# Performance work log

Hardware: AMD Instinct MI355X
Metric: run time of the kernel (lower is better)

Reference implementation:

```python
import jax, jax.numpy as jnp
import numpy as np

B, C, D, H, W = 2, 64, 12, 256, 64


def _conv1x1_relu(x, w, b):
    # x: (B, C, D, H, W); w: (C_out, C_in); b: (C_out,)
    y = jnp.einsum('oc,bcdhw->bodhw', w, x) + b[None, :, None, None, None]
    return jax.nn.relu(y)


def setup_inputs() -> dict:
    key = jax.random.key(0)
    ks = jax.random.split(key, 9)
    s = 1.0 / np.sqrt(C)
    inp = {
        'rep': jax.random.normal(ks[0], (B, C, D, H, W), dtype=jnp.float32),
        'Wq_w': jax.random.normal(ks[1], (C, C), dtype=jnp.float32) * s,
        'Wq_b': jnp.zeros((C,), dtype=jnp.float32),
        'Wk_w': jax.random.normal(ks[2], (C, C), dtype=jnp.float32) * s,
        'Wk_b': jnp.zeros((C,), dtype=jnp.float32),
        'Wv_w': jax.random.normal(ks[3], (C, C), dtype=jnp.float32) * s,
        'Wv_b': jnp.zeros((C,), dtype=jnp.float32),
        'FC_w': jax.random.normal(ks[4], (C, C), dtype=jnp.float32) * s,
        'FC_b': jnp.zeros((C,), dtype=jnp.float32),
    }
    return inp


def reference(rep, Wq_w, Wq_b, Wk_w, Wk_b, Wv_w, Wv_b, FC_w, FC_b):
    # 1x1x1 conv projections + ReLU, then permute to (B, D, W, H, C)
    q = _conv1x1_relu(rep, Wq_w, Wq_b).transpose(0, 2, 4, 3, 1)
    k = _conv1x1_relu(rep, Wk_w, Wk_b).transpose(0, 2, 4, 3, 1)
    v = _conv1x1_relu(rep, Wv_w, Wv_b).transpose(0, 2, 4, 3, 1)
    # attention over H axis: scores (B, D, W, H, H)
    scores = jnp.einsum('bdwhc,bdwgc->bdwhg', q, k) / jnp.sqrt(jnp.asarray(C, rep.dtype))
    attn = jax.nn.softmax(scores, axis=-1)
    out = jnp.einsum('bdwhg,bdwgc->bdwhc', attn, v)
    # permute(0,4,1,3,2): (B, D, W, H, C) -> (B, C, D, H, W)
    out = out.transpose(0, 4, 1, 3, 2)
    return _conv1x1_relu(out, FC_w, FC_b)
```

## Files before the change

kernel.cpp:

```cpp
#include <hip/hip_runtime.h>

typedef float f32x4 __attribute__((ext_vector_type(4)));
typedef short bf16x8 __attribute__((ext_vector_type(8)));
typedef unsigned short ushort_t;

#define NB 2
#define NC 64
#define ND 12
#define NH 256
#define NW 64
#define CSTRIDE (ND*NH*NW)
#define QSZ_ELEMS (24*64*256*64)
#define WS_NEED   ((size_t)3*QSZ_ELEMS*2)

__device__ __forceinline__ ushort_t bf_round(float f){
    unsigned int u = __float_as_uint(f);
    return (ushort_t)((u + 0x7fffu + ((u >> 16) & 1u)) >> 16);
}
__device__ __forceinline__ float bf_to_f(ushort_t s){ return __uint_as_float(((unsigned int)s) << 16); }

union U4S8 { uint4 u; bf16x8 s; };

__device__ __forceinline__ int row64_off(int r, int o){
    return r*128 + ((((o>>3) ^ (r&7)))<<4) + (o&7)*2;
}
__device__ __forceinline__ int row64_chunk(int r, int kchunk){
    return r*128 + (((kchunk ^ (r&7)))<<4);
}
__device__ __forceinline__ int vt_off(int c, int g){
    return c*512 + ((((g>>3) ^ (c&7)))<<4) + (g&7)*2;
}
__device__ __forceinline__ int vt_chunk(int c, int gchunk){
    return c*512 + (((gchunk ^ (c&7)))<<4);
}

__device__ __forceinline__ U4S8 wfrag_f(const float* W, int hl, int G, int ot, int m){
    const float* p2 = W + (hl + 16*ot)*NC + 32*m + 8*G;
    float4 f0 = *(const float4*)p2;
    float4 f1 = *(const float4*)(p2 + 4);
    U4S8 u; ushort_t* s = (ushort_t*)&u;
    s[0]=bf_round(f0.x); s[1]=bf_round(f0.y); s[2]=bf_round(f0.z); s[3]=bf_round(f0.w);
    s[4]=bf_round(f1.x); s[5]=bf_round(f1.y); s[6]=bf_round(f1.z); s[7]=bf_round(f1.w);
    return u;
}

__global__ __launch_bounds__(256, 2) void k1_proj(
    const float* __restrict__ rep,
    const float* __restrict__ Wq, const float* __restrict__ bq,
    const float* __restrict__ Wk, const float* __restrict__ bk,
    const float* __restrict__ Wv, const float* __restrict__ bv,
    ushort_t* __restrict__ qws, ushort_t* __restrict__ kws, ushort_t* __restrict__ vws)
{
    __shared__ __align__(16) unsigned char XL[32768];

    const int t = threadIdx.x, lane = t & 63, wid = t >> 6;
    const int G = lane >> 4, hl = lane & 15;
    const int blk = blockIdx.x;
    const int bd = blk >> 6;
    const int h0 = (blk & 63) * 4;
    const int d = bd % ND, b = bd / ND;
    const long dbase2 = (long)b*NC*CSTRIDE + (long)d*(NH*NW) + (long)h0*NW;

#pragma unroll
    for (int oct = 0; oct < 8; ++oct){
        float f[8];
#pragma unroll
        for (int j = 0; j < 8; ++j)
            f[j] = rep[dbase2 + (long)(8*oct + j)*CSTRIDE + t];
        U4S8 u; ushort_t* s = (ushort_t*)&u;
#pragma unroll
        for (int j = 0; j < 8; ++j) s[j] = bf_round(f[j]);
        *(uint4*)(XL + row64_chunk(t, oct)) = u.u;
    }
    __syncthreads();

    U4S8 xa[4][2];
#pragma unroll
    for (int nt = 0; nt < 4; ++nt)
#pragma unroll
        for (int m = 0; m < 2; ++m)
            xa[nt][m].u = *(const uint4*)(XL + row64_chunk(64*wid + 16*nt + hl, 4*m + G));
    __syncthreads();

    auto pass = [&](const float* W, const float* bias, float scale, ushort_t* dst){
        U4S8 bw[4][2];
        float bb[4];
#pragma unroll
        for (int ot = 0; ot < 4; ++ot){
            bw[ot][0] = wfrag_f(W, hl, G, ot, 0);
            bw[ot][1] = wfrag_f(W, hl, G, ot, 1);
            bb[ot] = bias[hl + 16*ot];
        }
        f32x4 acc[4][4];
#pragma unroll
        for (int nt = 0; nt < 4; ++nt)
#pragma unroll
            for (int ot = 0; ot < 4; ++ot){
                f32x4 a = {0.f,0.f,0.f,0.f};
                a = __builtin_amdgcn_mfma_f32_16x16x32_bf16(xa[nt][0].s, bw[ot][0].s, a, 0,0,0);
                a = __builtin_amdgcn_mfma_f32_16x16x32_bf16(xa[nt][1].s, bw[ot][1].s, a, 0,0,0);
#pragma unroll
                for (int r = 0; r < 4; ++r) a[r] = fmaxf(a[r] + bb[ot], 0.f) * scale;
                acc[nt][ot] = a;
            }
#pragma unroll
        for (int nt = 0; nt < 4; ++nt)
#pragma unroll
            for (int ot = 0; ot < 4; ++ot)
#pragma unroll
                for (int r = 0; r < 4; ++r){
                    int n = 64*wid + 16*nt + 4*G + r;
                    int o = hl + 16*ot;
                    *(ushort_t*)(XL + row64_off(n, o)) = bf_round(acc[nt][ot][r]);
                }
        __syncthreads();
#pragma unroll
        for (int i = 0; i < 8; ++i){
            int g2 = i*256 + t; int n = g2 >> 3; int c8 = g2 & 7;
            uint4 u = *(const uint4*)(XL + row64_chunk(n, c8));
            long row_g = ((long)bd*64 + (n & 63))*256 + h0 + (n >> 6);
            *(uint4*)((unsigned char*)dst + row_g*128 + c8*16) = u;
        }
        __syncthreads();
    };
    pass(Wq, bq, 0.125f, qws);
    pass(Wk, bk, 1.0f,   kws);
    pass(Wv, bv, 1.0f,   vws);
}

__global__ __launch_bounds__(256, 2) void k2_attn(
    ushort_t* __restrict__ qws, const ushort_t* __restrict__ kws, const ushort_t* __restrict__ vws)
{
    __shared__ __align__(16) unsigned char smem[65536];
    unsigned char* KL = smem;
    unsigned char* VT = smem + 32768;

    const int t = threadIdx.x, lane = t & 63, wid = t >> 6;
    const int G = lane >> 4, hl = lane & 15;
    const int bdw = blockIdx.x;
    ushort_t* qslice = qws + (size_t)bdw*16384;
    const unsigned char* kslice = (const unsigned char*)(kws + (size_t)bdw*16384);
    const unsigned char* vslice = (const unsigned char*)(vws + (size_t)bdw*16384);

#pragma unroll
    for (int i = 0; i < 8; ++i){
        int g2 = i*256 + t; int g = g2 >> 3; int c8 = g2 & 7;
        uint4 ku = *(const uint4*)(kslice + g2*16);
        *(uint4*)(KL + row64_chunk(g, c8)) = ku;
        U4S8 vu; vu.u = *(const uint4*)(vslice + g2*16);
#pragma unroll
        for (int j = 0; j < 8; ++j)
            *(ushort_t*)(VT + vt_off(8*c8 + j, g)) = (ushort_t)vu.s[j];
    }
    __syncthreads();

    U4S8 qfr[4][2];
#pragma unroll
    for (int ht = 0; ht < 4; ++ht)
#pragma unroll
        for (int m = 0; m < 2; ++m)
            qfr[ht][m].u = *(const uint4*)((const unsigned char*)qslice
                              + (64*wid + 16*ht + hl)*128 + (4*m + G)*16);

    f32x4 oacc[4][4];
#pragma unroll
    for (int ct = 0; ct < 4; ++ct)
#pragma unroll
        for (int ht = 0; ht < 4; ++ht) oacc[ct][ht] = (f32x4){0.f,0.f,0.f,0.f};
    float m_run[4], l_run[4];
#pragma unroll
    for (int ht = 0; ht < 4; ++ht){ m_run[ht] = -1e30f; l_run[ht] = 0.f; }

    const int srcq0 = (16*((2*G    ) & 3) + hl)*4;
    const int srcq1 = (16*((2*G + 1) & 3) + hl)*4;

    for (int gb = 0; gb < NH; gb += 64){
        U4S8 kfr[4][2];
#pragma unroll
        for (int gt = 0; gt < 4; ++gt)
#pragma unroll
            for (int m = 0; m < 2; ++m)
                kfr[gt][m].u = *(const uint4*)(KL + row64_chunk(gb + 16*gt + hl, 4*m + G));

        f32x4 sacc[4][4];
#pragma unroll
        for (int gt = 0; gt < 4; ++gt)
#pragma unroll
            for (int ht = 0; ht < 4; ++ht){
                f32x4 a = {0.f,0.f,0.f,0.f};
                a = __builtin_amdgcn_mfma_f32_16x16x32_bf16(kfr[gt][0].s, qfr[ht][0].s, a, 0,0,0);
                a = __builtin_amdgcn_mfma_f32_16x16x32_bf16(kfr[gt][1].s, qfr[ht][1].s, a, 0,0,0);
                sacc[gt][ht] = a;
            }

        unsigned int pk[4][4][2];
#pragma unroll
        for (int ht = 0; ht < 4; ++ht){
            float cm = -1e30f;
#pragma unroll
            for (int gt = 0; gt < 4; ++gt)
#pragma unroll
                for (int r = 0; r < 4; ++r) cm = fmaxf(cm, sacc[gt][ht][r]);
            cm = fmaxf(cm, __shfl_xor(cm, 16));
            cm = fmaxf(cm, __shfl_xor(cm, 32));
            const float mn  = fmaxf(m_run[ht], cm);
            const float corr = __expf(m_run[ht] - mn);
            m_run[ht] = mn;
            float ls = 0.f;
#pragma unroll
            for (int gt = 0; gt < 4; ++gt){
                f32x4 s = sacc[gt][ht];
                float e0 = __expf(s[0]-mn), e1 = __expf(s[1]-mn);
                float e2 = __expf(s[2]-mn), e3 = __expf(s[3]-mn);
                ls += (e0+e1)+(e2+e3);
                pk[ht][gt][0] = (unsigned int)bf_round(e0) | ((unsigned int)bf_round(e1) << 16);
                pk[ht][gt][1] = (unsigned int)bf_round(e2) | ((unsigned int)bf_round(e3) << 16);
            }
            ls += __shfl_xor(ls, 16);
            ls += __shfl_xor(ls, 32);
            l_run[ht] = l_run[ht]*corr + ls;
#pragma unroll
            for (int ct = 0; ct < 4; ++ct)
#pragma unroll
                for (int r = 0; r < 4; ++r) oacc[ct][ht][r] *= corr;
        }

        U4S8 vfr[4][2];
#pragma unroll
        for (int ct = 0; ct < 4; ++ct)
#pragma unroll
            for (int m = 0; m < 2; ++m)
                vfr[ct][m].u = *(const uint4*)(VT + vt_chunk(16*ct + hl, (gb>>3) + 4*m + G));

#pragma unroll
        for (int m = 0; m < 2; ++m){
            U4S8 bfr[4];
#pragma unroll
            for (int ht = 0; ht < 4; ++ht){
                unsigned int wv[4];
#pragma unroll
                for (int jj = 0; jj < 4; ++jj){
                    const int src = (jj >> 1) ? srcq1 : srcq0;
                    const int p2  = jj & 1;
                    int rA = __builtin_amdgcn_ds_bpermute(src, (int)pk[ht][2*m  ][p2]);
                    int rB = __builtin_amdgcn_ds_bpermute(src, (int)pk[ht][2*m+1][p2]);
                    wv[jj] = (lane < 32) ? (unsigned int)rA : (unsigned int)rB;
                }
                bfr[ht].u = make_uint4(wv[0], wv[1], wv[2], wv[3]);
            }
#pragma unroll
            for (int ct = 0; ct < 4; ++ct)
#pragma unroll
                for (int ht = 0; ht < 4; ++ht)
                    oacc[ct][ht] = __builtin_amdgcn_mfma_f32_16x16x32_bf16(vfr[ct][m].s, bfr[ht].s, oacc[ct][ht], 0,0,0);
        }
    }

    float invl[4];
#pragma unroll
    for (int ht = 0; ht < 4; ++ht) invl[ht] = 1.f / l_run[ht];

    __syncthreads();
#pragma unroll
    for (int ct = 0; ct < 4; ++ct)
#pragma unroll
        for (int ht = 0; ht < 4; ++ht)
#pragma unroll
            for (int r = 0; r < 4; ++r){
                int h = 64*wid + 16*ht + hl;
                int c = 16*ct + 4*G + r;
                *(ushort_t*)(KL + row64_off(h, c)) = bf_round(oacc[ct][ht][r] * invl[ht]);
            }
    __syncthreads();
#pragma unroll
    for (int i = 0; i < 8; ++i){
        int g2 = i*256 + t;
        uint4 u = *(const uint4*)(KL + row64_chunk(g2 >> 3, g2 & 7));
        *(uint4*)((unsigned char*)qslice + g2*16) = u;
    }
}

__global__ __launch_bounds__(256, 2) void k3_fc(
    const ushort_t* __restrict__ ows, const float* __restrict__ Wf, const float* __restrict__ bfc,
    float* __restrict__ out)
{
    __shared__ __align__(16) float YL[16384];

    const int t = threadIdx.x, lane = t & 63, wid = t >> 6;
    const int G = lane >> 4, hl = lane & 15;
    const int blk = blockIdx.x;
    const int bd = blk >> 6;
    const int h0 = (blk & 63) * 4;
    const int d = bd % ND, b = bd / ND;

    U4S8 xa[4][2];
#pragma unroll
    for (int nt = 0; nt < 4; ++nt)
#pragma unroll
        for (int m = 0; m < 2; ++m){
            long row_g = ((long)bd*64 + (16*nt + hl))*256 + h0 + wid;
            xa[nt][m].u = *(const uint4*)((const unsigned char*)ows + row_g*128 + (4*m + G)*16);
        }

    U4S8 bw[4][2];
    float bb[4];
#pragma unroll
    for (int ot = 0; ot < 4; ++ot){
        bw[ot][0] = wfrag_f(Wf, hl, G, ot, 0);
        bw[ot][1] = wfrag_f(Wf, hl, G, ot, 1);
        bb[ot] = bfc[hl + 16*ot];
    }

    f32x4 acc[4][4];
#pragma unroll
    for (int nt = 0; nt < 4; ++nt)
#pragma unroll
        for (int ot = 0; ot < 4; ++ot){
            f32x4 a = {0.f,0.f,0.f,0.f};
            a = __builtin_amdgcn_mfma_f32_16x16x32_bf16(xa[nt][0].s, bw[ot][0].s, a, 0,0,0);
            a = __builtin_amdgcn_mfma_f32_16x16x32_bf16(xa[nt][1].s, bw[ot][1].s, a, 0,0,0);
#pragma unroll
            for (int r = 0; r < 4; ++r) a[r] = fmaxf(a[r] + bb[ot], 0.f);
            acc[nt][ot] = a;
        }

#pragma unroll
    for (int nt = 0; nt < 4; ++nt)
#pragma unroll
        for (int ot = 0; ot < 4; ++ot)
#pragma unroll
            for (int r = 0; r < 4; ++r){
                int n = 64*wid + 16*nt + 4*G + r;
                int o = hl + 16*ot;
                YL[(n<<6) + (o ^ ((n>>2)&31))] = acc[nt][ot][r];
            }
    __syncthreads();

    const long base3 = (long)b*NC*CSTRIDE + (long)d*(NH*NW) + (long)h0*NW;
#pragma unroll
    for (int i = 0; i < 16; ++i){
        int idx = i*1024 + t*4;
        int o = idx >> 8;
        int n0 = idx & 255;
        int osw = o ^ (t & 31);
        float4 v;
        v.x = YL[((n0+0)<<6) + osw];
        v.y = YL[((n0+1)<<6) + osw];
        v.z = YL[((n0+2)<<6) + osw];
        v.w = YL[((n0+3)<<6) + osw];
        *(float4*)(&out[base3 + (long)o*CSTRIDE + n0]) = v;
    }
}

__global__ __launch_bounds__(256, 2) void sa_mfma(
    const float* __restrict__ rep,
    const float* __restrict__ Wq, const float* __restrict__ bq,
    const float* __restrict__ Wk, const float* __restrict__ bk,
    const float* __restrict__ Wv, const float* __restrict__ bv,
    const float* __restrict__ Wf, const float* __restrict__ bfc,
    float* __restrict__ out)
{
    __shared__ __align__(16) unsigned char smem[65536];
    unsigned char* BUFA = smem;
    unsigned char* BUFB = smem + 32768;

    const int t = threadIdx.x, lane = t & 63, wid = t >> 6;
    const int G = lane >> 4, hl = lane & 15;
    const int j = blockIdx.x;
    const int x = j & 7;
    const int p = j >> 3;
    const int group = ((p >> 6) << 3) + x;
    const int w = p & 63;
    const int d = group % ND;
    const int b = group / ND;
    const long base_bd = (long)b*(NC*CSTRIDE) + (long)d*(NH*NW) + w;

    {
        const int h = t;
        const long rbase = base_bd + (long)h*NW;
#pragma unroll
        for (int c8 = 0; c8 < 8; ++c8){
            U4S8 u;
            ushort_t* s = (ushort_t*)&u;
#pragma unroll
            for (int jj = 0; jj < 8; ++jj)
                s[jj] = bf_round(rep[rbase + (long)(c8*8 + jj)*CSTRIDE]);
            *(uint4*)(BUFB + row64_chunk(h, c8)) = u.u;
        }
    }
    U4S8 xafr[4][2];
#pragma unroll
    for (int ht = 0; ht < 4; ++ht)
#pragma unroll
        for (int m = 0; m < 2; ++m)
            xafr[ht][m].u = *(const uint4*)(BUFB + row64_chunk(64*wid + 16*ht + hl, 4*m + G));

    auto do_proj = [&](const float* W, const float* bias, float scale, f32x4 (&acc)[4][4]){
        U4S8 bw[4][2];
#pragma unroll
        for (int ot = 0; ot < 4; ++ot){ bw[ot][0] = wfrag_f(W, hl, G, ot, 0); bw[ot][1] = wfrag_f(W, hl, G, ot, 1); }
        float bb[4];
#pragma unroll
        for (int ot = 0; ot < 4; ++ot) bb[ot] = bias[hl + 16*ot];
#pragma unroll
        for (int ht = 0; ht < 4; ++ht)
#pragma unroll
            for (int ot = 0; ot < 4; ++ot){
                f32x4 a = {0.f, 0.f, 0.f, 0.f};
                a = __builtin_amdgcn_mfma_f32_16x16x32_bf16(xafr[ht][0].s, bw[ot][0].s, a, 0, 0, 0);
                a = __builtin_amdgcn_mfma_f32_16x16x32_bf16(xafr[ht][1].s, bw[ot][1].s, a, 0, 0, 0);
#pragma unroll
                for (int r = 0; r < 4; ++r) a[r] = fmaxf(a[r] + bb[ot], 0.f) * scale;
                acc[ht][ot] = a;
            }
    };

    {
        f32x4 qa[4][4];
        do_proj(Wq, bq, 0.125f, qa);
#pragma unroll
        for (int ht = 0; ht < 4; ++ht)
#pragma unroll
            for (int ot = 0; ot < 4; ++ot)
#pragma unroll
                for (int r = 0; r < 4; ++r){
                    int h = 64*wid + 16*ht + 4*G + r;
                    int o = hl + 16*ot;
                    *(ushort_t*)(BUFA + row64_off(h, o)) = bf_round(qa[ht][ot][r]);
                }
    }
    U4S8 qfr[4][2];
#pragma unroll
    for (int ht = 0; ht < 4; ++ht)
#pragma unroll
        for (int m = 0; m < 2; ++m)
            qfr[ht][m].u = *(const uint4*)(BUFA + row64_chunk(64*wid + 16*ht + hl, 4*m + G));

    {
        f32x4 ka[4][4];
        do_proj(Wk, bk, 1.0f, ka);
#pragma unroll
        for (int gt = 0; gt < 4; ++gt)
#pragma unroll
            for (int ot = 0; ot < 4; ++ot)
#pragma unroll
                for (int r = 0; r < 4; ++r){
                    int g = 64*wid + 16*gt + 4*G + r;
                    int o = hl + 16*ot;
                    *(ushort_t*)(BUFA + row64_off(g, o)) = bf_round(ka[gt][ot][r]);
                }
    }
    f32x4 va[4][4];
    do_proj(Wv, bv, 1.0f, va);
    __syncthreads();
#pragma unroll
    for (int gt = 0; gt < 4; ++gt)
#pragma unroll
        for (int ot = 0; ot < 4; ++ot)
#pragma unroll
            for (int r = 0; r < 4; ++r){
                int g = 64*wid + 16*gt + 4*G + r;
                int c = hl + 16*ot;
                *(ushort_t*)(BUFB + vt_off(c, g)) = bf_round(va[gt][ot][r]);
            }
    __syncthreads();

    f32x4 oacc[4][4];
#pragma unroll
    for (int ct = 0; ct < 4; ++ct)
#pragma unroll
        for (int ht = 0; ht < 4; ++ht) oacc[ct][ht] = (f32x4){0.f,0.f,0.f,0.f};
    float m_run[4], l_run[4];
#pragma unroll
    for (int ht = 0; ht < 4; ++ht){ m_run[ht] = -1e30f; l_run[ht] = 0.f; }

    const int srcq0 = (16*((2*G    ) & 3) + hl)*4;
    const int srcq1 = (16*((2*G + 1) & 3) + hl)*4;

    for (int gb = 0; gb < NH; gb += 64){
        U4S8 kfr[4][2];
#pragma unroll
        for (int gt = 0; gt < 4; ++gt)
#pragma unroll
            for (int m = 0; m < 2; ++m)
                kfr[gt][m].u = *(const uint4*)(BUFA + row64_chunk(gb + 16*gt + hl, 4*m + G));

        f32x4 sacc[4][4];
#pragma unroll
        for (int gt = 0; gt < 4; ++gt)
#pragma unroll
            for (int ht = 0; ht < 4; ++ht){
                f32x4 a = {0.f,0.f,0.f,0.f};
                a = __builtin_amdgcn_mfma_f32_16x16x32_bf16(kfr[gt][0].s, qfr[ht][0].s, a, 0,0,0);
                a = __builtin_amdgcn_mfma_f32_16x16x32_bf16(kfr[gt][1].s, qfr[ht][1].s, a, 0,0,0);
                sacc[gt][ht] = a;
            }

        unsigned int pk[4][4][2];
#pragma unroll
        for (int ht = 0; ht < 4; ++ht){
            float cm = -1e30f;
#pragma unroll
            for (int gt = 0; gt < 4; ++gt)
#pragma unroll
                for (int r = 0; r < 4; ++r) cm = fmaxf(cm, sacc[gt][ht][r]);
            cm = fmaxf(cm, __shfl_xor(cm, 16));
            cm = fmaxf(cm, __shfl_xor(cm, 32));
            const float mn  = fmaxf(m_run[ht], cm);
            const float corr = __expf(m_run[ht] - mn);
            m_run[ht] = mn;
            float ls = 0.f;
#pragma unroll
            for (int gt = 0; gt < 4; ++gt){
                f32x4 s = sacc[gt][ht];
                float e0 = __expf(s[0]-mn), e1 = __expf(s[1]-mn);
                float e2 = __expf(s[2]-mn), e3 = __expf(s[3]-mn);
                ls += (e0+e1)+(e2+e3);
                pk[ht][gt][0] = (unsigned int)bf_round(e0) | ((unsigned int)bf_round(e1) << 16);
                pk[ht][gt][1] = (unsigned int)bf_round(e2) | ((unsigned int)bf_round(e3) << 16);
            }
            ls += __shfl_xor(ls, 16);
            ls += __shfl_xor(ls, 32);
            l_run[ht] = l_run[ht]*corr + ls;
#pragma unroll
            for (int ct = 0; ct < 4; ++ct)
#pragma unroll
                for (int r = 0; r < 4; ++r) oacc[ct][ht][r] *= corr;
        }

        U4S8 vfr[4][2];
#pragma unroll
        for (int ct = 0; ct < 4; ++ct)
#pragma unroll
            for (int m = 0; m < 2; ++m)
                vfr[ct][m].u = *(const uint4*)(BUFB + vt_chunk(16*ct + hl, (gb>>3) + 4*m + G));

#pragma unroll
        for (int m = 0; m < 2; ++m){
            U4S8 bfr[4];
#pragma unroll
            for (int ht = 0; ht < 4; ++ht){
                unsigned int wv[4];
#pragma unroll
                for (int jj = 0; jj < 4; ++jj){
                    const int src = (jj >> 1) ? srcq1 : srcq0;
                    const int p2  = jj & 1;
                    int rA = __builtin_amdgcn_ds_bpermute(src, (int)pk[ht][2*m  ][p2]);
                    int rB = __builtin_amdgcn_ds_bpermute(src, (int)pk[ht][2*m+1][p2]);
                    wv[jj] = (lane < 32) ? (unsigned int)rA : (unsigned int)rB;
                }
                bfr[ht].u = make_uint4(wv[0], wv[1], wv[2], wv[3]);
            }
#pragma unroll
            for (int ct = 0; ct < 4; ++ct)
#pragma unroll
                for (int ht = 0; ht < 4; ++ht)
                    oacc[ct][ht] = __builtin_amdgcn_mfma_f32_16x16x32_bf16(vfr[ct][m].s, bfr[ht].s, oacc[ct][ht], 0,0,0);
        }
    }

    float invl[4];
#pragma unroll
    for (int ht = 0; ht < 4; ++ht) invl[ht] = 1.f / l_run[ht];
    __syncthreads();
#pragma unroll
    for (int ct = 0; ct < 4; ++ct)
#pragma unroll
        for (int ht = 0; ht < 4; ++ht)
#pragma unroll
            for (int r = 0; r < 4; ++r){
                float v = oacc[ct][ht][r] * invl[ht];
                ushort_t hi = bf_round(v);
                ushort_t lo = bf_round(v - bf_to_f(hi));
                int hrow = 64*wid + 16*ht + hl;
                int c = 16*ct + 4*G + r;
                *(ushort_t*)(BUFA + row64_off(hrow, c)) = hi;
                *(ushort_t*)(BUFB + row64_off(hrow, c)) = lo;
            }
    U4S8 bh[4][2], bl[4][2];
#pragma unroll
    for (int ht = 0; ht < 4; ++ht)
#pragma unroll
        for (int m = 0; m < 2; ++m){
            bh[ht][m].u = *(const uint4*)(BUFA + row64_chunk(64*wid + 16*ht + hl, 4*m + G));
            bl[ht][m].u = *(const uint4*)(BUFB + row64_chunk(64*wid + 16*ht + hl, 4*m + G));
        }

    f32x4 yacc[4][4];
#pragma unroll
    for (int ot = 0; ot < 4; ++ot)
#pragma unroll
        for (int ht = 0; ht < 4; ++ht) yacc[ot][ht] = (f32x4){0.f,0.f,0.f,0.f};
#pragma unroll
    for (int ot = 0; ot < 4; ++ot)
#pragma unroll
        for (int m = 0; m < 2; ++m){
            U4S8 wf = wfrag_f(Wf, hl, G, ot, m);
#pragma unroll
            for (int ht = 0; ht < 4; ++ht){
                yacc[ot][ht] = __builtin_amdgcn_mfma_f32_16x16x32_bf16(wf.s, bh[ht][m].s, yacc[ot][ht], 0,0,0);
                yacc[ot][ht] = __builtin_amdgcn_mfma_f32_16x16x32_bf16(wf.s, bl[ht][m].s, yacc[ot][ht], 0,0,0);
            }
        }
    float bfv[4][4];
#pragma unroll
    for (int ot = 0; ot < 4; ++ot)
#pragma unroll
        for (int r = 0; r < 4; ++r) bfv[ot][r] = bfc[16*ot + 4*G + r];
#pragma unroll
    for (int ot = 0; ot < 4; ++ot)
#pragma unroll
        for (int ht = 0; ht < 4; ++ht)
#pragma unroll
            for (int r = 0; r < 4; ++r){
                int o = 16*ot + 4*G + r;
                int h = 64*wid + 16*ht + hl;
                float y = fmaxf(yacc[ot][ht][r] + bfv[ot][r], 0.f);
                out[base_bd + (long)o*CSTRIDE + (long)h*NW] = y;
            }
}

extern "C" void kernel_launch(void* const* d_in, const int* in_sizes, int n_in,
                              void* d_out, int out_size, void* d_ws, size_t ws_size,
                              hipStream_t stream) {
    (void)in_sizes; (void)n_in; (void)out_size;
    const float* rep = (const float*)d_in[0];
    const float* Wq  = (const float*)d_in[1];
    const float* bq  = (const float*)d_in[2];
    const float* Wk  = (const float*)d_in[3];
    const float* bk  = (const float*)d_in[4];
    const float* Wv  = (const float*)d_in[5];
    const float* bv  = (const float*)d_in[6];
    const float* Wf  = (const float*)d_in[7];
    const float* bfc = (const float*)d_in[8];
    float* out = (float*)d_out;

    if (ws_size >= WS_NEED) {
        ushort_t* qws = (ushort_t*)d_ws;
        ushort_t* kws = qws + QSZ_ELEMS;
        ushort_t* vws = kws + QSZ_ELEMS;
        k1_proj<<<dim3(1536), dim3(256), 0, stream>>>(rep, Wq, bq, Wk, bk, Wv, bv, qws, kws, vws);
        k2_attn<<<dim3(1536), dim3(256), 0, stream>>>(qws, kws, vws);
        k3_fc  <<<dim3(1536), dim3(256), 0, stream>>>(qws, Wf, bfc, out);
    } else {
        sa_mfma<<<dim3(1536), dim3(256), 0, stream>>>(rep, Wq, bq, Wk, bk, Wv, bv, Wf, bfc, out);
    }
}
```

Before: 174.6 us.

## Double-buffer projection output staging and prefetch weights in projection kernel

The projection kernel now uses a second 32KB LDS buffer so each of the Q, K and V passes writes into an alternating bounce buffer. This drops the barrier between a pass's copy-out and the next pass's MFMA writes. Weight fragments for the next projection are loaded ahead of the current pass to hide global-load latency, and the MFMA epilogue writes straight to LDS without a separate accumulator array. In exchange, LDS per block doubles to 64KB and the occupancy hint in launch_bounds is removed, which may lower the number of resident blocks per CU.

After: 191.8 us. 1.1x slower.

```diff
diff --git a/kernel.cpp b/kernel.cpp
--- a/kernel.cpp
+++ b/kernel.cpp
@@ -44,7 +44,7 @@
     return u;
 }
 
-__global__ __launch_bounds__(256, 2) void k1_proj(
+__global__ __launch_bounds__(256) void k1_proj(
     const float* __restrict__ rep,
     const float* __restrict__ Wq, const float* __restrict__ bq,
     const float* __restrict__ Wk, const float* __restrict__ bk,
@@ -52,6 +52,7 @@
     ushort_t* __restrict__ qws, ushort_t* __restrict__ kws, ushort_t* __restrict__ vws)
 {
     __shared__ __align__(16) unsigned char XL[32768];
+    __shared__ __align__(16) unsigned char OB[32768];
 
     const int t = threadIdx.x, lane = t & 63, wid = t >> 6;
     const int G = lane >> 4, hl = lane & 15;
@@ -60,6 +61,15 @@
     const int h0 = (blk & 63) * 4;
     const int d = bd % ND, b = bd / ND;
     const long dbase2 = (long)b*NC*CSTRIDE + (long)d*(NH*NW) + (long)h0*NW;
+    const long wsrow0 = (long)bd*64*256 + h0;
+
+    U4S8 wqf[4][2]; float bbq[4];
+#pragma unroll
+    for (int ot = 0; ot < 4; ++ot){
+        wqf[ot][0] = wfrag_f(Wq, hl, G, ot, 0);
+        wqf[ot][1] = wfrag_f(Wq, hl, G, ot, 1);
+        bbq[ot] = bq[hl + 16*ot];
+    }
 
 #pragma unroll
     for (int oct = 0; oct < 8; ++oct){
@@ -80,18 +90,9 @@
 #pragma unroll
         for (int m = 0; m < 2; ++m)
             xa[nt][m].u = *(const uint4*)(XL + row64_chunk(64*wid + 16*nt + hl, 4*m + G));
-    __syncthreads();
-
-    auto pass = [&](const float* W, const float* bias, float scale, ushort_t* dst){
-        U4S8 bw[4][2];
-        float bb[4];
-#pragma unroll
-        for (int ot = 0; ot < 4; ++ot){
-            bw[ot][0] = wfrag_f(W, hl, G, ot, 0);
-            bw[ot][1] = wfrag_f(W, hl, G, ot, 1);
-            bb[ot] = bias[hl + 16*ot];
-        }
-        f32x4 acc[4][4];
+
+    auto mfma_pass = [&](U4S8 (&bw)[4][2], float (&bb)[4], float scale,
+                         unsigned char* bounce){
 #pragma unroll
         for (int nt = 0; nt < 4; ++nt)
 #pragma unroll
@@ -100,32 +101,50 @@
                 a = __builtin_amdgcn_mfma_f32_16x16x32_bf16(xa[nt][0].s, bw[ot][0].s, a, 0,0,0);
                 a = __builtin_amdgcn_mfma_f32_16x16x32_bf16(xa[nt][1].s, bw[ot][1].s, a, 0,0,0);
 #pragma unroll
-                for (int r = 0; r < 4; ++r) a[r] = fmaxf(a[r] + bb[ot], 0.f) * scale;
-                acc[nt][ot] = a;
-            }
-#pragma unroll
-        for (int nt = 0; nt < 4; ++nt)
-#pragma unroll
-            for (int ot = 0; ot < 4; ++ot)
-#pragma unroll
                 for (int r = 0; r < 4; ++r){
+                    float v = fmaxf(a[r] + bb[ot], 0.f) * scale;
                     int n = 64*wid + 16*nt + 4*G + r;
                     int o = hl + 16*ot;
-                    *(ushort_t*)(XL + row64_off(n, o)) = bf_round(acc[nt][ot][r]);
+                    *(ushort_t*)(bounce + row64_off(n, o)) = bf_round(v);
                 }
-        __syncthreads();
+            }
+    };
+    auto copyout = [&](const unsigned char* bounce, ushort_t* dst){
 #pragma unroll
         for (int i = 0; i < 8; ++i){
             int g2 = i*256 + t; int n = g2 >> 3; int c8 = g2 & 7;
-            uint4 u = *(const uint4*)(XL + row64_chunk(n, c8));
-            long row_g = ((long)bd*64 + (n & 63))*256 + h0 + (n >> 6);
+            uint4 u = *(const uint4*)(bounce + row64_chunk(n, c8));
+            long row_g = wsrow0 + (long)(n & 63)*256 + (n >> 6);
             *(uint4*)((unsigned char*)dst + row_g*128 + c8*16) = u;
         }
-        __syncthreads();
     };
-    pass(Wq, bq, 0.125f, qws);
-    pass(Wk, bk, 1.0f,   kws);
-    pass(Wv, bv, 1.0f,   vws);
+
+    U4S8 wkf[4][2]; float bbk[4];
+#pragma unroll
+    for (int ot = 0; ot < 4; ++ot){
+        wkf[ot][0] = wfrag_f(Wk, hl, G, ot, 0);
+        wkf[ot][1] = wfrag_f(Wk, hl, G, ot, 1);
+        bbk[ot] = bk[hl + 16*ot];
+    }
+    mfma_pass(wqf, bbq, 0.125f, OB);
+    __syncthreads();
+
+    copyout(OB, qws);
+    U4S8 wvf[4][2]; float bbv[4];
+#pragma unroll
+    for (int ot = 0; ot < 4; ++ot){
+        wvf[ot][0] = wfrag_f(Wv, hl, G, ot, 0);
+        wvf[ot][1] = wfrag_f(Wv, hl, G, ot, 1);
+        bbv[ot] = bv[hl + 16*ot];
+    }
+    mfma_pass(wkf, bbk, 1.0f, XL);
+    __syncthreads();
+
+    copyout(XL, kws);
+    mfma_pass(wvf, bbv, 1.0f, OB);
+    __syncthreads();
+
+    copyout(OB, vws);
 }
 
 __global__ __launch_bounds__(256, 2) void k2_attn(
```

## Split projection kernel into one block per Q/K/V pass with XCD-aware tile mapping

Applied to the files above, without the earlier changes.

The projection kernel now launches three times as many blocks, each computing only one of the Q, K or V projections for a tile instead of all three serially. Block indices are remapped so the three passes of the same tile land on the same XCD, which should let the repeated reads of the input tile hit in that XCD's L2. This adds parallelism and removes two rounds of barriers and LDS staging per block, at the cost of reading and converting the fp32 input three times per tile.

After: 174.8 us. Within noise of the previous version (+0.1%).

```diff
diff --git a/kernel.cpp b/kernel.cpp
--- a/kernel.cpp
+++ b/kernel.cpp
@@ -55,21 +55,41 @@
 
     const int t = threadIdx.x, lane = t & 63, wid = t >> 6;
     const int G = lane >> 4, hl = lane & 15;
-    const int blk = blockIdx.x;
-    const int bd = blk >> 6;
-    const int h0 = (blk & 63) * 4;
+
+    const int j = blockIdx.x;
+    const int xcd = j & 7;
+    const int pos = j >> 3;
+    const int tile = (pos / 3) * 8 + xcd;
+    const int pass = pos % 3;
+
+    const int bd = tile >> 6;
+    const int h0 = (tile & 63) * 4;
     const int d = bd % ND, b = bd / ND;
     const long dbase2 = (long)b*NC*CSTRIDE + (long)d*(NH*NW) + (long)h0*NW;
+    const long wsrow0 = (long)bd*64*256 + h0;
+
+    const float* W; const float* bias; ushort_t* dst; float scale;
+    if (pass == 0)      { W = Wq; bias = bq; dst = qws; scale = 0.125f; }
+    else if (pass == 1) { W = Wk; bias = bk; dst = kws; scale = 1.0f; }
+    else                { W = Wv; bias = bv; dst = vws; scale = 1.0f; }
+
+    U4S8 bw[4][2]; float bb[4];
+#pragma unroll
+    for (int ot = 0; ot < 4; ++ot){
+        bw[ot][0] = wfrag_f(W, hl, G, ot, 0);
+        bw[ot][1] = wfrag_f(W, hl, G, ot, 1);
+        bb[ot] = bias[hl + 16*ot];
+    }
 
 #pragma unroll
     for (int oct = 0; oct < 8; ++oct){
         float f[8];
 #pragma unroll
-        for (int j = 0; j < 8; ++j)
-            f[j] = rep[dbase2 + (long)(8*oct + j)*CSTRIDE + t];
+        for (int jj = 0; jj < 8; ++jj)
+            f[jj] = rep[dbase2 + (long)(8*oct + jj)*CSTRIDE + t];
         U4S8 u; ushort_t* s = (ushort_t*)&u;
 #pragma unroll
-        for (int j = 0; j < 8; ++j) s[j] = bf_round(f[j]);
+        for (int jj = 0; jj < 8; ++jj) s[jj] = bf_round(f[jj]);
         *(uint4*)(XL + row64_chunk(t, oct)) = u.u;
     }
     __syncthreads();
@@ -82,50 +102,30 @@
             xa[nt][m].u = *(const uint4*)(XL + row64_chunk(64*wid + 16*nt + hl, 4*m + G));
     __syncthreads();
 
-    auto pass = [&](const float* W, const float* bias, float scale, ushort_t* dst){
-        U4S8 bw[4][2];
-        float bb[4];
+#pragma unroll
+    for (int nt = 0; nt < 4; ++nt)
 #pragma unroll
         for (int ot = 0; ot < 4; ++ot){
-            bw[ot][0] = wfrag_f(W, hl, G, ot, 0);
-            bw[ot][1] = wfrag_f(W, hl, G, ot, 1);
-            bb[ot] = bias[hl + 16*ot];
-        }
-        f32x4 acc[4][4];
-#pragma unroll
-        for (int nt = 0; nt < 4; ++nt)
-#pragma unroll
-            for (int ot = 0; ot < 4; ++ot){
-                f32x4 a = {0.f,0.f,0.f,0.f};
-                a = __builtin_amdgcn_mfma_f32_16x16x32_bf16(xa[nt][0].s, bw[ot][0].s, a, 0,0,0);
-                a = __builtin_amdgcn_mfma_f32_16x16x32_bf16(xa[nt][1].s, bw[ot][1].s, a, 0,0,0);
-#pragma unroll
-                for (int r = 0; r < 4; ++r) a[r] = fmaxf(a[r] + bb[ot], 0.f) * scale;
-                acc[nt][ot] = a;
-            }
-#pragma unroll
-        for (int nt = 0; nt < 4; ++nt)
-#pragma unroll
-            for (int ot = 0; ot < 4; ++ot)
-#pragma unroll
-                for (int r = 0; r < 4; ++r){
-                    int n = 64*wid + 16*nt + 4*G + r;
-                    int o = hl + 16*ot;
-                    *(ushort_t*)(XL + row64_off(n, o)) = bf_round(acc[nt][ot][r]);
-                }
-        __syncthreads();
-#pragma unroll
-        for (int i = 0; i < 8; ++i){
-            int g2 = i*256 + t; int n = g2 >> 3; int c8 = g2 & 7;
-            uint4 u = *(const uint4*)(XL + row64_chunk(n, c8));
-            long row_g = ((long)bd*64 + (n & 63))*256 + h0 + (n >> 6);
-            *(uint4*)((unsigned char*)dst + row_g*128 + c8*16) = u;
-        }
-        __syncthreads();
-    };
-    pass(Wq, bq, 0.125f, qws);
-    pass(Wk, bk, 1.0f,   kws);
-    pass(Wv, bv, 1.0f,   vws);
+            f32x4 a = {0.f,0.f,0.f,0.f};
+            a = __builtin_amdgcn_mfma_f32_16x16x32_bf16(xa[nt][0].s, bw[ot][0].s, a, 0,0,0);
+            a = __builtin_amdgcn_mfma_f32_16x16x32_bf16(xa[nt][1].s, bw[ot][1].s, a, 0,0,0);
+#pragma unroll
+            for (int r = 0; r < 4; ++r){
+                float v = fmaxf(a[r] + bb[ot], 0.f) * scale;
+                int n = 64*wid + 16*nt + 4*G + r;
+                int o = hl + 16*ot;
+                *(ushort_t*)(XL + row64_off(n, o)) = bf_round(v);
+            }
+        }
+    __syncthreads();
+
+#pragma unroll
+    for (int i = 0; i < 8; ++i){
+        int g2 = i*256 + t; int n = g2 >> 3; int c8 = g2 & 7;
+        uint4 u = *(const uint4*)(XL + row64_chunk(n, c8));
+        long row_g = wsrow0 + (long)(n & 63)*256 + (n >> 6);
+        *(uint4*)((unsigned char*)dst + row_g*128 + c8*16) = u;
+    }
 }
 
 __global__ __launch_bounds__(256, 2) void k2_attn(
@@ -149,8 +149,8 @@
         *(uint4*)(KL + row64_chunk(g, c8)) = ku;
         U4S8 vu; vu.u = *(const uint4*)(vslice + g2*16);
 #pragma unroll
-        for (int j = 0; j < 8; ++j)
-            *(ushort_t*)(VT + vt_off(8*c8 + j, g)) = (ushort_t)vu.s[j];
+        for (int jj = 0; jj < 8; ++jj)
+            *(ushort_t*)(VT + vt_off(8*c8 + jj, g)) = (ushort_t)vu.s[jj];
     }
     __syncthreads();
 
@@ -639,7 +639,7 @@
         ushort_t* qws = (ushort_t*)d_ws;
         ushort_t* kws = qws + QSZ_ELEMS;
         ushort_t* vws = kws + QSZ_ELEMS;
-        k1_proj<<<dim3(1536), dim3(256), 0, stream>>>(rep, Wq, bq, Wk, bk, Wv, bv, qws, kws, vws);
+        k1_proj<<<dim3(4608), dim3(256), 0, stream>>>(rep, Wq, bq, Wk, bk, Wv, bv, qws, kws, vws);
         k2_attn<<<dim3(1536), dim3(256), 0, stream>>>(qws, kws, vws);
         k3_fc  <<<dim3(1536), dim3(256), 0, stream>>>(qws, Wf, bfc, out);
     } else {
```
